# Kernel tuning notes

Hardware: AMD Instinct MI355X
Metric: run time of the kernel (lower is better)

The kernel has to match this reference:

```python
import jax, jax.numpy as jnp
import numpy as np
from jax import lax

N = 1_000_000   # nodes
E = 16_000_000  # edges
K1, K2, K3 = 100_000, 10_000, 2_500  # ceil(ratio*n) per pooling stage
EPS = 1e-5


def cgconv(x, src, dst, edge_attr, edge_valid, Wf, bf, Ws, bs, gamma, beta, num_nodes):
    # z_ij = [x_i, x_j, e_ij]  (PyG: i = target = dst, j = source = src)
    z = jnp.concatenate([x[dst], x[src], edge_attr], axis=-1)          # [E,3]
    m = jax.nn.sigmoid(z @ Wf + bf) * jax.nn.softplus(z @ Ws + bs)     # [E,1]
    m = m * edge_valid[:, None].astype(m.dtype)
    aggr = jax.ops.segment_sum(m, dst, num_segments=num_nodes)         # [n,1]
    # BatchNorm1d (training-mode batch stats, biased var), then residual
    mean = aggr.mean(axis=0)
    var = aggr.var(axis=0)
    bn = gamma * (aggr - mean) / jnp.sqrt(var + EPS) + beta
    return bn + x


def topk_pool(x, src, dst, edge_attr, edge_valid, w, k, num_nodes):
    # Original torch code broadcasts x[N,1]*w[C] -> sum(-1) == x*sum(w); tanh nonlinearity.
    score = jnp.tanh(x[:, 0] * jnp.sum(w) / jnp.linalg.norm(w))        # [n]
    top_scores, perm = lax.top_k(score, k)
    x_new = x[perm] * top_scores[:, None]
    mask = jnp.zeros((num_nodes,), bool).at[perm].set(True)
    new_idx = jnp.zeros((num_nodes,), jnp.int32).at[perm].set(jnp.arange(k, dtype=jnp.int32))
    ev = edge_valid & mask[src] & mask[dst]
    return x_new, new_idx[src], new_idx[dst], edge_attr, ev


def setup_inputs() -> dict:
    key = jax.random.key(0)
    ks = jax.random.split(key, 24)
    d = {}
    d["x"] = jax.random.normal(ks[0], (N, 1), jnp.float32)
    d["edge_attr"] = jax.random.uniform(ks[1], (E, 1), jnp.float32)
    d["src"] = jax.random.randint(ks[2], (E,), 0, N, jnp.int32)
    d["dst"] = jax.random.randint(ks[3], (E,), 0, N, jnp.int32)
    d["batch"] = jnp.zeros((N,), jnp.int32)
    p = lambda k, shp: jax.random.normal(k, shp, jnp.float32) * 0.1
    d["Wf1"], d["bf1"] = p(ks[4], (3, 1)), p(ks[5], (1,))
    d["Ws1"], d["bs1"] = p(ks[6], (3, 1)), p(ks[7], (1,))
    d["g1"], d["be1"] = jnp.ones((1,), jnp.float32), jnp.zeros((1,), jnp.float32)
    d["Wf2"], d["bf2"] = p(ks[8], (3, 1)), p(ks[9], (1,))
    d["Ws2"], d["bs2"] = p(ks[10], (3, 1)), p(ks[11], (1,))
    d["g2"], d["be2"] = jnp.ones((1,), jnp.float32), jnp.zeros((1,), jnp.float32)
    d["pw1"] = p(ks[12], (800,))
    d["pw2"] = p(ks[13], (80,))
    d["pw3"] = p(ks[14], (8,))
    d["Wl1"], d["bl1"] = p(ks[15], (1, 8)), p(ks[16], (8,))
    d["Wl2"], d["bl2"] = p(ks[17], (8, 2)), p(ks[18], (2,))
    return d


def reference(x, edge_attr, Wf1, bf1, Ws1, bs1, g1, be1, Wf2, bf2, Ws2, bs2, g2, be2,
              pw1, pw2, pw3, Wl1, bl1, Wl2, bl2, src, dst, batch):
    ev = jnp.ones((E,), bool)
    x = cgconv(x, src, dst, edge_attr, ev, Wf1, bf1, Ws1, bs1, g1, be1, N)
    x, s, dd, ea, ev = topk_pool(x, src, dst, edge_attr, ev, pw1, K1, N)
    x = cgconv(x, s, dd, ea, ev, Wf2, bf2, Ws2, bs2, g2, be2, K1)
    x, s, dd, ea, ev = topk_pool(x, s, dd, ea, ev, pw2, K2, K1)
    x, s, dd, ea, ev = topk_pool(x, s, dd, ea, ev, pw3, K3, K2)
    h = jax.nn.relu(x @ Wl1 + bl1)
    # dropout is identity in eval/reference mode
    return jax.nn.log_softmax(h @ Wl2 + bl2, axis=1)
```

## Files before the change

### kernel.cpp

```cpp
#include <hip/hip_runtime.h>
#include <math.h>

#define CHUNK 4096
#define NB2   256
#define BSH   12
#define CAP   24
#define CAPW  49
#define FG    16
#define RND   1024
#define EPB   16384

typedef int      i32x4 __attribute__((ext_vector_type(4)));
typedef float    f32x4 __attribute__((ext_vector_type(4)));
typedef unsigned u32x2 __attribute__((ext_vector_type(2)));
typedef unsigned u32x4 __attribute__((ext_vector_type(4)));

__device__ __forceinline__ i32x4 ntld4i(const int* p)   { return __builtin_nontemporal_load((const i32x4*)p); }
__device__ __forceinline__ f32x4 ntld4f(const float* p) { return __builtin_nontemporal_load((const f32x4*)p); }

__device__ __forceinline__ float sigmoidf_(float x) {
    if (x >= 0.0f) { float e = expf(-x); return 1.0f / (1.0f + e); }
    float e = expf(x); return e / (1.0f + e);
}
__device__ __forceinline__ float softplusf_(float x) {
    return fmaxf(x, 0.0f) + log1pf(expf(-fabsf(x)));
}
__device__ __forceinline__ unsigned key_desc(float f) {
    unsigned u = __float_as_uint(f);
    unsigned ka = (u & 0x80000000u) ? ~u : (u | 0x80000000u);
    return ~ka;
}
__device__ __forceinline__ float edge_m(float xd, float xs, float a,
                                        float wf0, float wf1, float wf2, float b0,
                                        float ws0, float ws1, float ws2, float b1) {
    float f = xd * wf0 + xs * wf1 + a * wf2 + b0;
    float g = xd * ws0 + xs * ws1 + a * ws2 + b1;
    return sigmoidf_(f) * softplusf_(g);
}

__global__ void k_consts(const float* __restrict__ pw1, const float* __restrict__ pw2,
                         const float* __restrict__ pw3, float* __restrict__ consts,
                         float* __restrict__ stats, unsigned* __restrict__ ghist,
                         int n1, int n2, int n3) {
    if (blockIdx.x == 0) {
        if (threadIdx.x < 16) stats[threadIdx.x] = 0.f;
        for (int i = threadIdx.x; i < 2048; i += 256) ghist[i] = 0u;
    }
    const float* w; int n;
    if (blockIdx.x == 0)      { w = pw1; n = n1; }
    else if (blockIdx.x == 1) { w = pw2; n = n2; }
    else                      { w = pw3; n = n3; }
    __shared__ float s1[256], s2[256];
    float a = 0.f, b = 0.f;
    for (int i = threadIdx.x; i < n; i += 256) { float v = w[i]; a += v; b += v * v; }
    s1[threadIdx.x] = a; s2[threadIdx.x] = b; __syncthreads();
    for (int o = 128; o > 0; o >>= 1) {
        if (threadIdx.x < o) { s1[threadIdx.x] += s1[threadIdx.x + o]; s2[threadIdx.x] += s2[threadIdx.x + o]; }
        __syncthreads();
    }
    if (threadIdx.x == 0) consts[blockIdx.x] = s1[0] / sqrtf(s2[0]);
}

__global__ void __launch_bounds__(256) k_ehist2(const int* __restrict__ dst,
                                                unsigned* __restrict__ hist,
                                                int e0, int e1) {
    __shared__ unsigned h[NB2];
    int t = threadIdx.x;
    h[t] = 0;
    __syncthreads();
    int cs = e0 + blockIdx.x * EPB;
    int ce = cs + EPB; if (ce > e1) ce = e1;
    for (int eb = cs; eb < ce; eb += RND) {
        int i = eb + t * 4;
        if (eb + RND <= ce) {
            i32x4 d4 = ntld4i(dst + i);
            atomicAdd(&h[((unsigned)d4.x) >> BSH], 1u);
            atomicAdd(&h[((unsigned)d4.y) >> BSH], 1u);
            atomicAdd(&h[((unsigned)d4.z) >> BSH], 1u);
// ... 130 lines not shown
    }
    for (int i = 0; i < NB2 / 16; ++i) {
        int b = sg + (i << 4);
        unsigned g = gcur[b], c = fil[b], ge = gend[b];
        unsigned* st = &stage[b * CAPW];
        for (unsigned p = g + ln; p < ge; p += 16) {
            unsigned k2 = p - g;
            rec[p] = (k2 < c) ? make_uint2(st[2 * k2], st[2 * k2 + 1]) : make_uint2(0u, 0u);
        }
    }
}

__global__ void __launch_bounds__(256) k_aggr2(
        const uint2* __restrict__ rec, const unsigned* __restrict__ tot,
        float* __restrict__ aggr, float* __restrict__ stats,
        int N, int accumulate, int doStats) {
    __shared__ float acc[1 << BSH];
    __shared__ unsigned sc[256];
    __shared__ unsigned sBase, sCnt;
    int t = threadIdx.x, b = blockIdx.x;
    {
        unsigned v = tot[t];
        sc[t] = v; __syncthreads();
        for (int o = 1; o < 256; o <<= 1) {
            unsigned u = (t >= o) ? sc[t - o] : 0u;
            __syncthreads();
            sc[t] += u; __syncthreads();
        }
        if (t == b) { sBase = sc[t] - v; sCnt = tot[t]; }
    }
    for (int i = t; i < (1 << BSH); i += 256) acc[i] = 0.f;
    __syncthreads();
    unsigned lo = sBase, hi = lo + sCnt;
    for (unsigned i = lo + t; i < hi; i += 256) {
        u32x2 r = __builtin_nontemporal_load((const u32x2*)&rec[i]);
        atomicAdd(&acc[r.y], __uint_as_float(r.x));
    }
    __syncthreads();
    int nb = b << BSH;
    float s = 0.f, q = 0.f;
    for (int i = t; i < (1 << BSH); i += 256) {
        int node = nb + i;
        if (node < N) {
            float v = acc[i];
            if (accumulate) v += aggr[node];
            aggr[node] = v;
            if (doStats) { s += v; q += v * v; }
        }
    }
    if (doStats) {
        __shared__ float s1[256], s2[256];
        s1[t] = s; s2[t] = q; __syncthreads();
        for (int o = 128; o > 0; o >>= 1) {
            if (t < o) { s1[t] += s1[t + o]; s2[t] += s2[t + o]; }
            __syncthreads();
        }
        if (t == 0) { atomicAdd(&stats[0], s1[0]); atomicAdd(&stats[1], s2[0]); }
    }
}

__global__ void k_conv1(const float* __restrict__ x, const float* __restrict__ ea,
                        const int* __restrict__ src, const int* __restrict__ dst,
                        const float* __restrict__ Wf, const float* __restrict__ bf,
                        const float* __restrict__ Ws, const float* __restrict__ bs,
                        float* __restrict__ aggr, int E) {
    int e = blockIdx.x * blockDim.x + threadIdx.x;
    if (e >= E) return;
    int s = src[e], d = dst[e];
    atomicAdd(&aggr[d], edge_m(x[d], x[s], ea[e], Wf[0], Wf[1], Wf[2], bf[0],
// ... 19 lines not shown
        s4[0]=sv.x; s4[1]=sv.y; s4[2]=sv.z; s4[3]=sv.w;
        cnt = 4;
    } else {
        cnt = E - base;
        for (int j = 0; j < cnt; ++j) { d4[j] = dst[base + j]; s4[j] = src[base + j]; }
    }
    #pragma unroll
    for (int j = 0; j < 4; ++j) {
        if (j >= cnt) break;
        int nd = nidx[d4[j]];
        if (nd < 0) continue;
        int ns = nidx[s4[j]];
        if (ns < 0) continue;
        float a = __builtin_nontemporal_load(ea + base + j);
        atomicAdd(&aggr[nd], edge_m(x2[nd], x2[ns], a, wf0, wf1, wf2, b0, ws0, ws1, ws2, b1));
    }
}

__global__ void k_stats(const float* __restrict__ a, int n, float* __restrict__ stats) {
    float s = 0.f, q = 0.f;
    int stride = gridDim.x * blockDim.x;
    for (int i = blockIdx.x * blockDim.x + threadIdx.x; i < n; i += stride) {
        float v = a[i]; s += v; q += v * v;
    }
    __shared__ float s1[256], s2[256];
    s1[threadIdx.x] = s; s2[threadIdx.x] = q; __syncthreads();
    for (int o = 128; o > 0; o >>= 1) {
        if (threadIdx.x < o) { s1[threadIdx.x] += s1[threadIdx.x + o]; s2[threadIdx.x] += s2[threadIdx.x + o]; }
        __syncthreads();
    }
    if (threadIdx.x == 0) { atomicAdd(&stats[0], s1[0]); atomicAdd(&stats[1], s2[0]); }
}

__global__ void k_bn(const float* __restrict__ aggr, const float* __restrict__ xin,
                     const float* __restrict__ stats, const float* __restrict__ g,
                     const float* __restrict__ be, float* __restrict__ xout,
                     int n, float invn, const float* __restrict__ consts, int ci,
                     unsigned* __restrict__ keys, unsigned* __restrict__ vals,
                     int* __restrict__ nidxInit, float* __restrict__ zeroArr, int nZero) {
    int i = blockIdx.x * blockDim.x + threadIdx.x;
    if (i >= n) return;
    if (nidxInit) nidxInit[i] = -1;
    if (zeroArr && i < nZero) zeroArr[i] = 0.f;
    float mean = stats[0] * invn;
    float var  = stats[1] * invn - mean * mean;
    float inv  = 1.0f / sqrtf(var + 1e-5f);
    float v = g[0] * (aggr[i] - mean) * inv + be[0] + xin[i];
    xout[i] = v;
    float s = tanhf(v * consts[ci]);
    keys[i] = key_desc(s);
    vals[i] = (unsigned)i;
}

__global__ void __launch_bounds__(256) k_ghist(const unsigned* __restrict__ keys,
                                               unsigned* __restrict__ ghist, int n) {
    __shared__ unsigned h[2048];
    int t = threadIdx.x;
    for (int i = t; i < 2048; i += 256) h[i] = 0;
    __syncthreads();
    int stride = gridDim.x * 1024;
    for (int base = blockIdx.x * 1024 + t * 4; base + 3 < n; base += stride) {
        u32x4 k4 = __builtin_nontemporal_load((const u32x4*)(keys + base));
        atomicAdd(&h[k4.x >> 21], 1u);
        atomicAdd(&h[k4.y >> 21], 1u);
        atomicAdd(&h[k4.z >> 21], 1u);
        atomicAdd(&h[k4.w >> 21], 1u);
    }
    if (blockIdx.x == 0) {
        int tail = n & ~3;
        for (int i = tail + t; i < n; i += 256)
            atomicAdd(&h[keys[i] >> 21], 1u);
    }
    __syncthreads();
    for (int i = t; i < 2048; i += 256) { unsigned v = h[i]; if (v) atomicAdd(&ghist[i], v); }
}

__global__ void k_findT(const unsigned* __restrict__ ghist, unsigned* __restrict__ sel, int K) {
    __shared__ unsigned s[256];
    int t = threadIdx.x;
    unsigned carry = 0;
    for (int tile = 0; tile < 8; ++tile) {
        unsigned v = ghist[tile * 256 + t];
        s[t] = v; __syncthreads();
        for (int o = 1; o < 256; o <<= 1) {
            unsigned u = (t >= o) ? s[t - o] : 0u;
            __syncthreads();
            s[t] += u; __syncthreads();
        }
        unsigned cum = s[t] + carry;
        if (cum >= (unsigned)K && cum - v < (unsigned)K) {
            sel[0] = (unsigned)(tile * 256 + t);
            sel[1] = cum;
        }
        unsigned tl = s[255]; __syncthreads();
        carry += tl;
    }
}

__global__ void __launch_bounds__(256) k_selcnt(const unsigned* __restrict__ keys,
                                                const unsigned* __restrict__ sel,
                                                unsigned* __restrict__ chist, int n) {
    unsigned T = sel[0];
    int t = threadIdx.x;
    int base = blockIdx.x * CHUNK;
    int end = base + CHUNK; if (end > n) end = n;
    unsigned c = 0;
    for (int i = base + t; i < end; i += 256)
        c += ((keys[i] >> 21) <= T) ? 1u : 0u;
    __shared__ unsigned s[256];
    s[t] = c; __syncthreads();
    for (int o = 128; o > 0; o >>= 1) { if (t < o) s[t] += s[t + o]; __syncthreads(); }
    if (t == 0) chist[blockIdx.x] = s[0];
}

__global__ void __launch_bounds__(256) k_selcompact(
        const unsigned* __restrict__ keys, const unsigned* __restrict__ vals,
        const unsigned* __restrict__ sel, const unsigned* __restrict__ chist,
        unsigned* __restrict__ okeys, unsigned* __restrict__ ovals, int n, int G) {
    __shared__ unsigned s[256];
    __shared__ unsigned wsum[4];
    __shared__ unsigned runS;
    unsigned T = sel[0];
    int t = threadIdx.x, wave = t >> 6, lane = t & 63;
    unsigned v = (t < G) ? chist[t] : 0u;
    s[t] = v; __syncthreads();
    for (int o = 1; o < 256; o <<= 1) {
        unsigned u = (t >= o) ? s[t - o] : 0u;
        __syncthreads();
        s[t] += u; __syncthreads();
    }
    if (t == (int)blockIdx.x) runS = s[t] - v;
    __syncthreads();
    int cbase = blockIdx.x * CHUNK;
    for (int gix = 0; gix < CHUNK / 256; ++gix) {
        int i = cbase + gix * 256 + t;
        bool selq = (i < n) && ((keys[i] >> 21) <= T);
        unsigned long long mk = __ballot(selq);
        unsigned pre = (unsigned)__popcll(mk & ((1ull << lane) - 1ull));
        if (lane == 0) wsum[wave] = (unsigned)__popcll(mk);
        __syncthreads();
        unsigned wb = runS;
        #pragma unroll
        for (int w = 0; w < 4; ++w) if (w < wave) wb += wsum[w];
        if (selq) { unsigned pos = wb + pre; okeys[pos] = keys[i]; ovals[pos] = vals[i]; }
        __syncthreads();
        if (t == 0) runS += wsum[0] + wsum[1] + wsum[2] + wsum[3];
        __syncthreads();
    }
}

__global__ void k_hist(const unsigned* __restrict__ keys, unsigned* __restrict__ hist,
                       int n, const unsigned* __restrict__ pn, int shift) {
    if (pn) n = (int)*pn;
    __shared__ unsigned h[256];
    int t = threadIdx.x;
    h[t] = 0;
    __syncthreads();
    int base = blockIdx.x * CHUNK;
    if (base + CHUNK <= n) {
        #pragma unroll
        for (int it = 0; it < CHUNK / 1024; ++it) {
            int i = base + it * 1024 + t * 4;
            const unsigned* p = keys + i;
            unsigned k0 = p[0], k1 = p[1], k2 = p[2], k3 = p[3];
            atomicAdd(&h[(k0 >> shift) & 255u], 1u);
            atomicAdd(&h[(k1 >> shift) & 255u], 1u);
            atomicAdd(&h[(k2 >> shift) & 255u], 1u);
            atomicAdd(&h[(k3 >> shift) & 255u], 1u);
        }
    } else {
        for (int i = base + t; i < n; i += 256)
            atomicAdd(&h[(keys[i] >> shift) & 255u], 1u);
    }
    __syncthreads();
    hist[blockIdx.x * 256 + t] = h[t];
}

__global__ void __launch_bounds__(256) k_scatter(const unsigned* __restrict__ keys,
                                                 const unsigned* __restrict__ vals,
                                                 unsigned* __restrict__ okeys,
                                                 unsigned* __restrict__ ovals,
                                                 const unsigned* __restrict__ offs,
                                                 const unsigned* __restrict__ tot,
                                                 int n, const unsigned* __restrict__ pn,
                                                 int shift) {
    if (pn) n = (int)*pn;
    if ((int)blockIdx.x * CHUNK >= n) return;
    __shared__ unsigned run[256];
    __shared__ unsigned offl[256];
    __shared__ unsigned wcnt[4][256];
    __shared__ unsigned wpre[4][256];
    __shared__ unsigned sc[256];
    int t = threadIdx.x;
    int wave = t >> 6, lane = t & 63;
    {
        unsigned v = tot[t];
        sc[t] = v; __syncthreads();
        for (int o = 1; o < 256; o <<= 1) {
            unsigned u = (t >= o) ? sc[t - o] : 0u;
            __syncthreads();
            sc[t] += u; __syncthreads();
        }
        offl[t] = offs[(size_t)blockIdx.x * 256 + t] + (sc[t] - v);
        run[t] = 0;
    }
    __syncthreads();
    int cbase = blockIdx.x * CHUNK;
    const int GROUPS = CHUNK / 256;
    for (int gix = 0; gix < GROUPS; ++gix) {
        int i = cbase + gix * 256 + t;
        bool active = i < n;
        unsigned k = active ? keys[i] : 0u;
        unsigned v = active ? vals[i] : 0u;
        unsigned d = (k >> shift) & 255u;
        unsigned long long amask = __ballot(active);
        unsigned long long bb[8];
        #pragma unroll
        for (int bit = 0; bit < 8; ++bit) bb[bit] = __ballot(active && ((d >> bit) & 1u));
        unsigned long long m = amask;
        #pragma unroll
        for (int bit = 0; bit < 8; ++bit) m &= ((d >> bit) & 1u) ? bb[bit] : ~bb[bit];
        unsigned rk = (unsigned)__popcll(m & ((1ull << lane) - 1ull));
        #pragma unroll
        for (int j = 0; j < 4; ++j) {
            unsigned dd = (unsigned)lane + j * 64u;
            unsigned long long mm = amask;
            #pragma unroll
            for (int bit = 0; bit < 8; ++bit) mm &= ((dd >> bit) & 1u) ? bb[bit] : ~bb[bit];
            wcnt[wave][dd] = (unsigned)__popcll(mm);
        }
        __syncthreads();
        {
            unsigned r = run[t];
            unsigned c0 = wcnt[0][t], c1 = wcnt[1][t], c2 = wcnt[2][t], c3 = wcnt[3][t];
            wpre[0][t] = r;
            wpre[1][t] = r + c0;
            wpre[2][t] = r + c0 + c1;
            wpre[3][t] = r + c0 + c1 + c2;
            run[t] = r + c0 + c1 + c2 + c3;
        }
        __syncthreads();
        if (active) {
            unsigned pos = offl[d] + wpre[wave][d] + rk;
            okeys[pos] = k;
            ovals[pos] = v;
        }
    }
}

__global__ void k_pool(const unsigned* __restrict__ perm, const float* __restrict__ xin,
                       const float* __restrict__ consts, int ci,
                       float* __restrict__ xout, int* __restrict__ newidx, int k,
                       unsigned* __restrict__ okeys, unsigned* __restrict__ ovals, int nci) {
    int r = blockIdx.x * blockDim.x + threadIdx.x;
    if (r >= k) return;
    unsigned p = perm[r];
    float xv = xin[p];
    float s = tanhf(xv * consts[ci]);
    float o = xv * s;
    xout[r] = o;
    if (newidx) newidx[p] = r;
    if (okeys) {
        float s2 = tanhf(o * consts[nci]);
        okeys[r] = key_desc(s2);
        ovals[r] = (unsigned)r;
    }
}

__global__ void __launch_bounds__(1024) k_smallsort(
        unsigned* __restrict__ kIn, unsigned* __restrict__ vIn,
        unsigned* __restrict__ kTmp, unsigned* __restrict__ vTmp,
        int n, int k3, const float* __restrict__ xin,
        const float* __restrict__ consts, int ci,
        const float* __restrict__ Wl1, const float* __restrict__ bl1,
        const float* __restrict__ Wl2, const float* __restrict__ bl2,
        float* __restrict__ out) {
    __shared__ unsigned hist[256], sc[256], run[256], offl[256];
    __shared__ unsigned wcnt[16][256];
    __shared__ unsigned wpre[16][256];
    int t = threadIdx.x;
    int wave = t >> 6, lane = t & 63;
    unsigned *ki = kIn, *vi = vIn, *ko = kTmp, *vo = vTmp;
    for (int p = 0; p < 4; ++p) {
        int shift = p * 8;
        if (t < 256) hist[t] = 0;
        __syncthreads();
        for (int i = t; i < n; i += 1024)
            atomicAdd(&hist[(ki[i] >> shift) & 255u], 1u);
        __syncthreads();
        if (t < 256) sc[t] = hist[t];
        __syncthreads();
        for (int o = 1; o < 256; o <<= 1) {
            unsigned u = 0;
            if (t < 256 && t >= o) u = sc[t - o];
            __syncthreads();
            if (t < 256) sc[t] += u;
            __syncthreads();
        }
// ... 33 lines not shown
            if (active) {
                unsigned pos = offl[d] + wpre[wave][d] + rk;
                ko[pos] = k;
                vo[pos] = v;
            }
            __syncthreads();
        }
        unsigned* tp;
        tp = ki; ki = ko; ko = tp;
        tp = vi; vi = vo; vo = tp;
        __syncthreads();
    }
    float c = consts[ci];
    float b20 = bl2[0], b21 = bl2[1];
    for (int r = t; r < k3; r += 1024) {
        unsigned pidx = vIn[r];
        float xv = xin[pidx];
        float s = tanhf(xv * c);
        float o = xv * s;
        float l0 = b20, l1 = b21;
        #pragma unroll
        for (int j = 0; j < 8; ++j) {
            float h = fmaxf(o * Wl1[j] + bl1[j], 0.0f);
            l0 += h * Wl2[2 * j];
            l1 += h * Wl2[2 * j + 1];
        }
        float mx = fmaxf(l0, l1);
        float lse = mx + logf(expf(l0 - mx) + expf(l1 - mx));
        out[2 * r]     = l0 - lse;
        out[2 * r + 1] = l1 - lse;
    }
}

static void sort_pairs(hipStream_t stream, unsigned* kI, unsigned* vI,
                       unsigned* kT, unsigned* vT, unsigned* hist, unsigned* offs,
                       unsigned* tot, int n, int G, const unsigned* pn) {
    unsigned *ki = kI, *vi = vI, *ko = kT, *vo = vT;
    for (int p = 0; p < 4; ++p) {
        int shift = p * 8;
        k_hist<<<G, 256, 0, stream>>>(ki, hist, n, pn, shift);
        k_scanA<<<256, 256, 0, stream>>>(hist, offs, tot, G, 0u);
        k_scatter<<<G, 256, 0, stream>>>(ki, vi, ko, vo, offs, tot, n, pn, shift);
        unsigned* t;
        t = ki; ki = ko; ko = t;
        t = vi; vi = vo; vo = t;
    }
}

extern "C" void kernel_launch(void* const* d_in, const int* in_sizes, int n_in,
                              void* d_out, int out_size, void* d_ws, size_t ws_size,
                              hipStream_t stream) {
    const float* x   = (const float*)d_in[0];
    const float* ea  = (const float*)d_in[1];
    const int*   src = (const int*)d_in[2];
    const int*   dst = (const int*)d_in[3];
    const float *Wf1 = (const float*)d_in[5],  *bf1 = (const float*)d_in[6];
    const float *Ws1 = (const float*)d_in[7],  *bs1 = (const float*)d_in[8];
    const float *g1  = (const float*)d_in[9],  *be1 = (const float*)d_in[10];
    const float *Wf2 = (const float*)d_in[11], *bf2 = (const float*)d_in[12];
    const float *Ws2 = (const float*)d_in[13], *bs2 = (const float*)d_in[14];
    const float *g2  = (const float*)d_in[15], *be2 = (const float*)d_in[16];
    const float *pw1 = (const float*)d_in[17], *pw2 = (const float*)d_in[18], *pw3 = (const float*)d_in[19];
    const float *Wl1 = (const float*)d_in[20], *bl1 = (const float*)d_in[21];
    const float *Wl2 = (const float*)d_in[22], *bl2 = (const float*)d_in[23];

    const int N  = in_sizes[0];
    const int E  = in_sizes[1];
    const int K1 = 100000, K2 = 10000, K3 = 2500;

    size_t off = 0;
    auto alloc = [&](size_t bytes) { size_t o = off; off = (off + bytes + 255) & ~(size_t)255; return o; };
    char* ws = (char*)d_ws;
    size_t o_x1    = alloc((size_t)N * 4);
    size_t o_nidx  = alloc((size_t)N * 4);
    size_t o_stats = alloc(256);
    size_t o_const = alloc(256);
    size_t o_tot   = alloc(4096);
    size_t o_gh    = alloc(8192);
    size_t o_x2    = alloc((size_t)K1 * 4);
    size_t o_x3    = alloc((size_t)K1 * 4);
    size_t o_ag2   = alloc((size_t)K1 * 4);
    size_t o_x4    = alloc((size_t)K2 * 4);
    size_t o_ag1   = alloc((size_t)N * 4);
    size_t o_arena = off;

    int G1 = (N + CHUNK - 1) / CHUNK;
    size_t s_kA = 0;
    size_t s_vA = s_kA + (((size_t)N * 4 + 255) & ~(size_t)255);
    size_t s_kB = s_vA + (((size_t)N * 4 + 255) & ~(size_t)255);
    size_t s_vB = s_kB + (((size_t)N * 4 + 255) & ~(size_t)255);
    size_t s_h  = s_vB + (((size_t)N * 4 + 255) & ~(size_t)255);
    size_t s_o  = s_h  + (((size_t)G1 * 256 * 4 + 255) & ~(size_t)255);
    size_t sortSz = s_o + (size_t)G1 * 256 * 4;

    int H = 0, Eh = 0;
    size_t p_rec = 0, p_eh = 0, p_eo = 0;
    for (int h = 1; h <= 8; h <<= 1) {
        int eh_ = (E + h - 1) / h;
        eh_ = (eh_ + RND - 1) & ~(RND - 1);
        int gc_ = (eh_ + EPB - 1) / EPB;
        size_t recB = (((size_t)eh_ + (size_t)gc_ * NB2 * FG + NB2 * FG) * 8 + 255) & ~(size_t)255;
        size_t ehB  = (((size_t)gc_ * NB2 * 4) + 255) & ~(size_t)255;
        size_t eoB  = (((size_t)gc_ * NB2 * 4) + 255) & ~(size_t)255;
        size_t partSz = recB + ehB + eoB;
        size_t arenaSz = partSz > sortSz ? partSz : sortSz;
        if (o_arena + arenaSz <= ws_size && N <= (NB2 << BSH)) {
            H = h; Eh = eh_;
            p_rec = 0; p_eh = p_rec + recB; p_eo = p_eh + ehB;
            break;
        }
    }

    float*    x1     = (float*)(ws + o_x1);
    int*      nidx   = (int*)(ws + o_nidx);
    float*    stats  = (float*)(ws + o_stats);
    float*    consts = (float*)(ws + o_const);
    unsigned* tot    = (unsigned*)(ws + o_tot);
    unsigned* selp   = tot + 512;
    unsigned* ghist  = (unsigned*)(ws + o_gh);
    float*    x2     = (float*)(ws + o_x2);
    float*    x3     = (float*)(ws + o_x3);
    float*    aggr2  = (float*)(ws + o_ag2);
    float*    x4     = (float*)(ws + o_x4);
    float*    aggr1  = (float*)(ws + o_ag1);
    unsigned* kA     = (unsigned*)(ws + o_arena + s_kA);
    unsigned* vA     = (unsigned*)(ws + o_arena + s_vA);
    unsigned* kB     = (unsigned*)(ws + o_arena + s_kB);
    unsigned* vB     = (unsigned*)(ws + o_arena + s_vB);
    unsigned* hist   = (unsigned*)(ws + o_arena + s_h);
    unsigned* offs   = (unsigned*)(ws + o_arena + s_o);

    k_consts<<<3, 256, 0, stream>>>(pw1, pw2, pw3, consts, stats, ghist,
                                    in_sizes[17], in_sizes[18], in_sizes[19]);

    if (H > 0) {
        uint2*    rec = (uint2*)(ws + o_arena + p_rec);
        unsigned* eh  = (unsigned*)(ws + o_arena + p_eh);
        unsigned* eo  = (unsigned*)(ws + o_arena + p_eo);
        int NBN = (N + (1 << BSH) - 1) >> BSH;
        for (int h = 0; h < H; ++h) {
            int e0 = h * Eh;
            int e1 = e0 + Eh; if (e1 > E) e1 = E;
            if (e0 >= e1) break;
            int GCh = (e1 - e0 + EPB - 1) / EPB;
            k_ehist2<<<GCh, 256, 0, stream>>>(dst, eh, e0, e1);
            k_scanA<<<NB2, 256, 0, stream>>>(eh, eo, tot, GCh, (unsigned)(FG - 1));
            k_part<<<GCh, 256, 0, stream>>>(x, ea, src, dst, Wf1, bf1, Ws1, bs1,
                                            eo, tot, eh, rec, e0, e1);
            k_aggr2<<<NBN, 256, 0, stream>>>(rec, tot, aggr1, stats, N,
                                             h > 0, h == H - 1 ? 1 : 0);
        }
    } else {
        hipMemsetAsync(aggr1, 0, (size_t)N * 4, stream);
        k_conv1<<<(E + 255) / 256, 256, 0, stream>>>(x, ea, src, dst, Wf1, bf1, Ws1, bs1, aggr1, E);
        k_stats<<<1024, 256, 0, stream>>>(aggr1, N, stats);
    }
    k_bn<<<(N + 255) / 256, 256, 0, stream>>>(aggr1, x, stats, g1, be1, x1, N, 1.0f / (float)N,
                                              consts, 0, kA, vA, nidx, aggr2, K1);

    k_ghist<<<256, 256, 0, stream>>>(kA, ghist, N);
    k_findT<<<1, 256, 0, stream>>>(ghist, selp, K1);
    k_selcnt<<<G1, 256, 0, stream>>>(kA, selp, hist, N);
    k_selcompact<<<G1, 256, 0, stream>>>(kA, vA, selp, hist, kB, vB, N, G1);
    sort_pairs(stream, kB, vB, kA, vA, hist, offs, tot, N, G1, selp + 1);
    k_pool<<<(K1 + 255) / 256, 256, 0, stream>>>(vB, x1, consts, 0, x2, nidx, K1,
                                                 (unsigned*)nullptr, (unsigned*)nullptr, 0);

    k_conv2<<<(E / 4 + 255) / 256, 256, 0, stream>>>(x2, ea, src, dst, nidx,
                                                     Wf2, bf2, Ws2, bs2, aggr2, E);
    k_stats<<<256, 256, 0, stream>>>(aggr2, K1, stats + 2);
    k_bn<<<(K1 + 255) / 256, 256, 0, stream>>>(aggr2, x2, stats + 2, g2, be2, x3, K1, 1.0f / (float)K1,
                                               consts, 1, kA, vA,
                                               (int*)nullptr, (float*)nullptr, 0);

    sort_pairs(stream, kA, vA, kB, vB, hist, offs, tot, K1,
               (K1 + CHUNK - 1) / CHUNK, (const unsigned*)nullptr);
    k_pool<<<(K2 + 255) / 256, 256, 0, stream>>>(vA, x3, consts, 1, x4, (int*)nullptr, K2,
                                                 kB, vB, 2);

    k_smallsort<<<1, 1024, 0, stream>>>(kB, vB, kA, vA, K2, K3, x4, consts, 2,
                                        Wl1, bl1, Wl2, bl2, (float*)d_out);
}
```

Before: 845.7 us.

## Fuse selection and radix sort passes into persistent kernels with grid barriers

Replaces the chain of small launches (batch norm, global histogram, threshold find, select count, compaction, and four hist/scan/scatter radix passes plus pooling) with three persistent kernels that synchronise through a software grid barrier built on atomics. Each sort block now computes its digit offsets by reading every block's histogram directly, which removes the separate scan kernel and the offs buffer. It also changes the bucket capacity constants and has the aggregation loop read two records per 16-byte load. The aim is to cut launch overhead and inter-kernel gaps. In exchange it relies on all blocks of each grid being resident at once, since otherwise the spin barrier deadlocks, and each sort pass now does a redundant per-block sweep over all block histograms.

```diff
diff --git a/kernel.cpp b/kernel.cpp
--- a/kernel.cpp
+++ b/kernel.cpp
@@ -4,8 +4,8 @@
 #define CHUNK 4096
 #define NB2   256
 #define BSH   12
-#define CAP   24
-#define CAPW  49
+#define CAP   20
+#define CAPW  41
 #define FG    16
 #define RND   1024
 #define EPB   16384
@@ -38,12 +38,28 @@
     return sigmoidf_(f) * softplusf_(g);
 }
 
+__device__ __forceinline__ void gridbar(unsigned* cnt, unsigned* ep, unsigned G) {
+    __syncthreads();
+    __threadfence();
+    if (threadIdx.x == 0) {
+        __hip_atomic_fetch_add(cnt, 1u, __ATOMIC_ACQ_REL, __HIP_MEMORY_SCOPE_AGENT);
+        unsigned tgt = (*ep + 1u) * G;
+        while (__hip_atomic_load(cnt, __ATOMIC_ACQUIRE, __HIP_MEMORY_SCOPE_AGENT) < tgt)
+            __builtin_amdgcn_s_sleep(8);
+    }
+    ++(*ep);
+    __syncthreads();
+    __threadfence();
+}
+
 __global__ void k_consts(const float* __restrict__ pw1, const float* __restrict__ pw2,
                          const float* __restrict__ pw3, float* __restrict__ consts,
                          float* __restrict__ stats, unsigned* __restrict__ ghist,
+                         unsigned* __restrict__ cnts,
                          int n1, int n2, int n3) {
     if (blockIdx.x == 0) {
         if (threadIdx.x < 16) stats[threadIdx.x] = 0.f;
+        if (threadIdx.x < 8)  cnts[threadIdx.x] = 0u;
         for (int i = threadIdx.x; i < 2048; i += 256) ghist[i] = 0u;
     }
     const float* w; int n;
@@ -240,9 +256,10 @@
     for (int i = t; i < (1 << BSH); i += 256) acc[i] = 0.f;
     __syncthreads();
     unsigned lo = sBase, hi = lo + sCnt;
-    for (unsigned i = lo + t; i < hi; i += 256) {
-        u32x2 r = __builtin_nontemporal_load((const u32x2*)&rec[i]);
+    for (unsigned i = lo + 2 * t; i < hi; i += 512) {
+        u32x4 r = __builtin_nontemporal_load((const u32x4*)&rec[i]);
         atomicAdd(&acc[r.y], __uint_as_float(r.x));
+        atomicAdd(&acc[r.w], __uint_as_float(r.z));
     }
     __syncthreads();
     int nb = b << BSH;
@@ -328,238 +345,252 @@
     if (threadIdx.x == 0) { atomicAdd(&stats[0], s1[0]); atomicAdd(&stats[1], s2[0]); }
 }
 
-__global__ void k_bn(const float* __restrict__ aggr, const float* __restrict__ xin,
-                     const float* __restrict__ stats, const float* __restrict__ g,
-                     const float* __restrict__ be, float* __restrict__ xout,
-                     int n, float invn, const float* __restrict__ consts, int ci,
-                     unsigned* __restrict__ keys, unsigned* __restrict__ vals,
-                     int* __restrict__ nidxInit, float* __restrict__ zeroArr, int nZero) {
-    int i = blockIdx.x * blockDim.x + threadIdx.x;
-    if (i >= n) return;
-    if (nidxInit) nidxInit[i] = -1;
-    if (zeroArr && i < nZero) zeroArr[i] = 0.f;
-    float mean = stats[0] * invn;
-    float var  = stats[1] * invn - mean * mean;
-    float inv  = 1.0f / sqrtf(var + 1e-5f);
-    float v = g[0] * (aggr[i] - mean) * inv + be[0] + xin[i];
-    xout[i] = v;
-    float s = tanhf(v * consts[ci]);
-    keys[i] = key_desc(s);
-    vals[i] = (unsigned)i;
-}
-
-__global__ void __launch_bounds__(256) k_ghist(const unsigned* __restrict__ keys,
-                                               unsigned* __restrict__ ghist, int n) {
-    __shared__ unsigned h[2048];
-    int t = threadIdx.x;
-    for (int i = t; i < 2048; i += 256) h[i] = 0;
-    __syncthreads();
-    int stride = gridDim.x * 1024;
-    for (int base = blockIdx.x * 1024 + t * 4; base + 3 < n; base += stride) {
-        u32x4 k4 = __builtin_nontemporal_load((const u32x4*)(keys + base));
-        atomicAdd(&h[k4.x >> 21], 1u);
-        atomicAdd(&h[k4.y >> 21], 1u);
-        atomicAdd(&h[k4.z >> 21], 1u);
-        atomicAdd(&h[k4.w >> 21], 1u);
-    }
-    if (blockIdx.x == 0) {
-        int tail = n & ~3;
-        for (int i = tail + t; i < n; i += 256)
-            atomicAdd(&h[keys[i] >> 21], 1u);
-    }
-    __syncthreads();
-    for (int i = t; i < 2048; i += 256) { unsigned v = h[i]; if (v) atomicAdd(&ghist[i], v); }
-}
-
-__global__ void k_findT(const unsigned* __restrict__ ghist, unsigned* __restrict__ sel, int K) {
-    __shared__ unsigned s[256];
-    int t = threadIdx.x;
-    unsigned carry = 0;
-    for (int tile = 0; tile < 8; ++tile) {
-        unsigned v = ghist[tile * 256 + t];
-        s[t] = v; __syncthreads();
-        for (int o = 1; o < 256; o <<= 1) {
-            unsigned u = (t >= o) ? s[t - o] : 0u;
-            __syncthreads();
-            s[t] += u; __syncthreads();
-        }
-        unsigned cum = s[t] + carry;
-        if (cum >= (unsigned)K && cum - v < (unsigned)K) {
-            sel[0] = (unsigned)(tile * 256 + t);
-            sel[1] = cum;
-        }
-        unsigned tl = s[255]; __syncthreads();
-        carry += tl;
-    }
-}
-
-__global__ void __launch_bounds__(256) k_selcnt(const unsigned* __restrict__ keys,
-                                                const unsigned* __restrict__ sel,
-                                                unsigned* __restrict__ chist, int n) {
-    unsigned T = sel[0];
-    int t = threadIdx.x;
-    int base = blockIdx.x * CHUNK;
-    int end = base + CHUNK; if (end > n) end = n;
-    unsigned c = 0;
-    for (int i = base + t; i < end; i += 256)
-        c += ((keys[i] >> 21) <= T) ? 1u : 0u;
-    __shared__ unsigned s[256];
-    s[t] = c; __syncthreads();
-    for (int o = 128; o > 0; o >>= 1) { if (t < o) s[t] += s[t + o]; __syncthreads(); }
-    if (t == 0) chist[blockIdx.x] = s[0];
-}
-
-__global__ void __launch_bounds__(256) k_selcompact(
-        const unsigned* __restrict__ keys, const unsigned* __restrict__ vals,
-        const unsigned* __restrict__ sel, const unsigned* __restrict__ chist,
-        unsigned* __restrict__ okeys, unsigned* __restrict__ ovals, int n, int G) {
-    __shared__ unsigned s[256];
+__global__ void __launch_bounds__(256) k_select(
+        const float* __restrict__ aggr1, const float* __restrict__ x,
+        const float* __restrict__ stats, const float* __restrict__ g1,
+        const float* __restrict__ be1, const float* __restrict__ consts,
+        float* __restrict__ x1, unsigned* __restrict__ keys, unsigned* __restrict__ vals,
+        int* __restrict__ nidx, float* __restrict__ aggr2, int K1, int N, float invn,
+        unsigned* __restrict__ ghist, unsigned* __restrict__ sel,
+        unsigned* __restrict__ chist, unsigned* __restrict__ okeys,
+        unsigned* __restrict__ ovals, unsigned* __restrict__ cnt, int Gc) {
+    __shared__ unsigned h2[2048];
+    __shared__ unsigned fs[256];
     __shared__ unsigned wsum[4];
     __shared__ unsigned runS;
+    unsigned ep = 0;
+    int t = threadIdx.x, b = blockIdx.x;
+    unsigned G = gridDim.x;
+    for (int i = t; i < 2048; i += 256) h2[i] = 0;
+    __syncthreads();
+    {
+        float mean = stats[0] * invn;
+        float var  = stats[1] * invn - mean * mean;
+        float rinv = 1.0f / sqrtf(var + 1e-5f);
+        float gg = g1[0], bb = be1[0], c0 = consts[0];
+        int gid = b * 256 + t, gsz = (int)G * 256;
+        for (int i = gid; i < N; i += gsz) {
+            float v = gg * (aggr1[i] - mean) * rinv + bb + x[i];
+            x1[i] = v;
+            unsigned k = key_desc(tanhf(v * c0));
+            keys[i] = k;
+            vals[i] = (unsigned)i;
+            nidx[i] = -1;
+            if (i < K1) aggr2[i] = 0.f;
+            atomicAdd(&h2[k >> 21], 1u);
+        }
+    }
+    __syncthreads();
+    for (int i = t; i < 2048; i += 256) { unsigned v = h2[i]; if (v) atomicAdd(&ghist[i], v); }
+    gridbar(cnt, &ep, G);
+    if (b == 0) {
+        unsigned carry = 0;
+        int K = K1;
+        for (int tile = 0; tile < 8; ++tile) {
+            unsigned v = ghist[tile * 256 + t];
+            fs[t] = v; __syncthreads();
+            for (int o = 1; o < 256; o <<= 1) {
+                unsigned u = (t >= o) ? fs[t - o] : 0u;
+                __syncthreads();
+                fs[t] += u; __syncthreads();
+            }
+            unsigned cum = fs[t] + carry;
+            if (cum >= (unsigned)K && cum - v < (unsigned)K) {
+                sel[0] = (unsigned)(tile * 256 + t);
+                sel[1] = cum;
+            }
+            unsigned tl = fs[255]; __syncthreads();
+            carry += tl;
+        }
+    }
+    gridbar(cnt, &ep, G);
     unsigned T = sel[0];
-    int t = threadIdx.x, wave = t >> 6, lane = t & 63;
-    unsigned v = (t < G) ? chist[t] : 0u;
-    s[t] = v; __syncthreads();
-    for (int o = 1; o < 256; o <<= 1) {
-        unsigned u = (t >= o) ? s[t - o] : 0u;
-        __syncthreads();
-        s[t] += u; __syncthreads();
-    }
-    if (t == (int)blockIdx.x) runS = s[t] - v;
-    __syncthreads();
-    int cbase = blockIdx.x * CHUNK;
-    for (int gix = 0; gix < CHUNK / 256; ++gix) {
-        int i = cbase + gix * 256 + t;
-        bool selq = (i < n) && ((keys[i] >> 21) <= T);
-        unsigned long long mk = __ballot(selq);
-        unsigned pre = (unsigned)__popcll(mk & ((1ull << lane) - 1ull));
-        if (lane == 0) wsum[wave] = (unsigned)__popcll(mk);
-        __syncthreads();
-        unsigned wb = runS;
-        #pragma unroll
-        for (int w = 0; w < 4; ++w) if (w < wave) wb += wsum[w];
-        if (selq) { unsigned pos = wb + pre; okeys[pos] = keys[i]; ovals[pos] = vals[i]; }
-        __syncthreads();
-        if (t == 0) runS += wsum[0] + wsum[1] + wsum[2] + wsum[3];
-        __syncthreads();
-    }
-}
-
-__global__ void k_hist(const unsigned* __restrict__ keys, unsigned* __restrict__ hist,
-                       int n, const unsigned* __restrict__ pn, int shift) {
-    if (pn) n = (int)*pn;
-    __shared__ unsigned h[256];
-    int t = threadIdx.x;
-    h[t] = 0;
-    __syncthreads();
-    int base = blockIdx.x * CHUNK;
-    if (base + CHUNK <= n) {
-        #pragma unroll
-        for (int it = 0; it < CHUNK / 1024; ++it) {
-            int i = base + it * 1024 + t * 4;
-            const unsigned* p = keys + i;
-            unsigned k0 = p[0], k1 = p[1], k2 = p[2], k3 = p[3];
-            atomicAdd(&h[(k0 >> shift) & 255u], 1u);
-            atomicAdd(&h[(k1 >> shift) & 255u], 1u);
-            atomicAdd(&h[(k2 >> shift) & 255u], 1u);
-            atomicAdd(&h[(k3 >> shift) & 255u], 1u);
-        }
-    } else {
-        for (int i = base + t; i < n; i += 256)
-            atomicAdd(&h[(keys[i] >> shift) & 255u], 1u);
-    }
-    __syncthreads();
-    hist[blockIdx.x * 256 + t] = h[t];
-}
-
-__global__ void __launch_bounds__(256) k_scatter(const unsigned* __restrict__ keys,
-                                                 const unsigned* __restrict__ vals,
-                                                 unsigned* __restrict__ okeys,
-                                                 unsigned* __restrict__ ovals,
-                                                 const unsigned* __restrict__ offs,
-                                                 const unsigned* __restrict__ tot,
-                                                 int n, const unsigned* __restrict__ pn,
-                                                 int shift) {
-    if (pn) n = (int)*pn;
-    if ((int)blockIdx.x * CHUNK >= n) return;
-    __shared__ unsigned run[256];
-    __shared__ unsigned offl[256];
-    __shared__ unsigned wcnt[4][256];
-    __shared__ unsigned wpre[4][256];
-    __shared__ unsigned sc[256];
-    int t = threadIdx.x;
+    if (b < Gc) {
+        int base = b * CHUNK;
+        int end = base + CHUNK; if (end > N) end = N;
+        unsigned c = 0;
+        for (int i = base + t; i < end; i += 256)
+            c += ((keys[i] >> 21) <= T) ? 1u : 0u;
+        fs[t] = c; __syncthreads();
+        for (int o = 128; o > 0; o >>= 1) { if (t < o) fs[t] += fs[t + o]; __syncthreads(); }
+        if (t == 0) chist[b] = fs[0];
+    }
+    gridbar(cnt, &ep, G);
+    if (b < Gc) {
+        unsigned partial = 0;
+        for (int g = t; g < b; g += 256) partial += chist[g];
+        fs[t] = partial; __syncthreads();
+        for (int o = 128; o > 0; o >>= 1) { if (t < o) fs[t] += fs[t + o]; __syncthreads(); }
+        if (t == 0) runS = fs[0];
+        __syncthreads();
+        int wave = t >> 6, lane = t & 63;
+        int cbase = b * CHUNK;
+        for (int gix = 0; gix < CHUNK / 256; ++gix) {
+            int i = cbase + gix * 256 + t;
+            bool selq = (i < N) && ((keys[i] >> 21) <= T);
+            unsigned long long mk = __ballot(selq);
+            unsigned pre = (unsigned)__popcll(mk & ((1ull << lane) - 1ull));
+            if (lane == 0) wsum[wave] = (unsigned)__popcll(mk);
+            __syncthreads();
+            unsigned wb = runS;
+            #pragma unroll
+            for (int w = 0; w < 4; ++w) if (w < wave) wb += wsum[w];
+            if (selq) { unsigned pos = wb + pre; okeys[pos] = keys[i]; ovals[pos] = vals[i]; }
+            __syncthreads();
+            if (t == 0) runS += wsum[0] + wsum[1] + wsum[2] + wsum[3];
+            __syncthreads();
+        }
+    }
+}
+
+__device__ __forceinline__ void msort_body(unsigned*& ki, unsigned*& vi,
+                                           unsigned*& ko, unsigned*& vo,
+                                           int n, unsigned* hist,
+                                           unsigned* cnt, unsigned* ep) {
+    __shared__ unsigned h[256], offl[256], run[256], sc[256];
+    __shared__ unsigned wcnt[4][256], wpre[4][256];
+    int t = threadIdx.x, b = blockIdx.x;
+    unsigned G = gridDim.x;
     int wave = t >> 6, lane = t & 63;
-    {
-        unsigned v = tot[t];
-        sc[t] = v; __syncthreads();
+    for (int p = 0; p < 4; ++p) {
+        int shift = p * 8;
+        h[t] = 0;
+        __syncthreads();
+        int base = b * CHUNK;
+        if (base + CHUNK <= n) {
+            #pragma unroll
+            for (int it = 0; it < CHUNK / 1024; ++it) {
+                int i = base + it * 1024 + t * 4;
+                const unsigned* pk = ki + i;
+                atomicAdd(&h[(pk[0] >> shift) & 255u], 1u);
+                atomicAdd(&h[(pk[1] >> shift) & 255u], 1u);
+                atomicAdd(&h[(pk[2] >> shift) & 255u], 1u);
+                atomicAdd(&h[(pk[3] >> shift) & 255u], 1u);
+            }
+        } else {
+            for (int i = base + t; i < n; i += 256)
+                atomicAdd(&h[(ki[i] >> shift) & 255u], 1u);
+        }
+        __syncthreads();
+        hist[(size_t)b * 256 + t] = h[t];
+        gridbar(cnt, ep, G);
+        unsigned pre = 0, totd = 0;
+        for (int g = 0; g < (int)G; ++g) {
+            unsigned v = hist[(size_t)g * 256 + t];
+            pre += (g < b) ? v : 0u;
+            totd += v;
+        }
+        sc[t] = totd; __syncthreads();
         for (int o = 1; o < 256; o <<= 1) {
             unsigned u = (t >= o) ? sc[t - o] : 0u;
             __syncthreads();
             sc[t] += u; __syncthreads();
         }
-        offl[t] = offs[(size_t)blockIdx.x * 256 + t] + (sc[t] - v);
+        offl[t] = (sc[t] - totd) + pre;
         run[t] = 0;
-    }
-    __syncthreads();
-    int cbase = blockIdx.x * CHUNK;
-    const int GROUPS = CHUNK / 256;
-    for (int gix = 0; gix < GROUPS; ++gix) {
-        int i = cbase + gix * 256 + t;
-        bool active = i < n;
-        unsigned k = active ? keys[i] : 0u;
-        unsigned v = active ? vals[i] : 0u;
-        unsigned d = (k >> shift) & 255u;
-        unsigned long long amask = __ballot(active);
-        unsigned long long bb[8];
-        #pragma unroll
-        for (int bit = 0; bit < 8; ++bit) bb[bit] = __ballot(active && ((d >> bit) & 1u));
-        unsigned long long m = amask;
-        #pragma unroll
-        for (int bit = 0; bit < 8; ++bit) m &= ((d >> bit) & 1u) ? bb[bit] : ~bb[bit];
-        unsigned rk = (unsigned)__popcll(m & ((1ull << lane) - 1ull));
-        #pragma unroll
-        for (int j = 0; j < 4; ++j) {
-            unsigned dd = (unsigned)lane + j * 64u;
-            unsigned long long mm = amask;
-            #pragma unroll
-            for (int bit = 0; bit < 8; ++bit) mm &= ((dd >> bit) & 1u) ? bb[bit] : ~bb[bit];
-            wcnt[wave][dd] = (unsigned)__popcll(mm);
-        }
-        __syncthreads();
-        {
-            unsigned r = run[t];
-            unsigned c0 = wcnt[0][t], c1 = wcnt[1][t], c2 = wcnt[2][t], c3 = wcnt[3][t];
-            wpre[0][t] = r;
-            wpre[1][t] = r + c0;
-            wpre[2][t] = r + c0 + c1;
-            wpre[3][t] = r + c0 + c1 + c2;
-            run[t] = r + c0 + c1 + c2 + c3;
-        }
-        __syncthreads();
-        if (active) {
-            unsigned pos = offl[d] + wpre[wave][d] + rk;
-            okeys[pos] = k;
-            ovals[pos] = v;
-        }
-    }
-}
-
-__global__ void k_pool(const unsigned* __restrict__ perm, const float* __restrict__ xin,
-                       const float* __restrict__ consts, int ci,
-                       float* __restrict__ xout, int* __restrict__ newidx, int k,
-                       unsigned* __restrict__ okeys, unsigned* __restrict__ ovals, int nci) {
-    int r = blockIdx.x * blockDim.x + threadIdx.x;
-    if (r >= k) return;
-    unsigned p = perm[r];
-    float xv = xin[p];
-    float s = tanhf(xv * consts[ci]);
-    float o = xv * s;
-    xout[r] = o;
-    if (newidx) newidx[p] = r;
-    if (okeys) {
-        float s2 = tanhf(o * consts[nci]);
-        okeys[r] = key_desc(s2);
-        ovals[r] = (unsigned)r;
+        __syncthreads();
+        if (base < n) {
+            for (int gix = 0; gix < CHUNK / 256; ++gix) {
+                int i = base + gix * 256 + t;
+                bool active = i < n;
+                unsigned k = active ? ki[i] : 0u;
+                unsigned v = active ? vi[i] : 0u;
+                unsigned d = (k >> shift) & 255u;
+                unsigned long long amask = __ballot(active);
+                unsigned long long bb[8];
+                #pragma unroll
+                for (int bit = 0; bit < 8; ++bit) bb[bit] = __ballot(active && ((d >> bit) & 1u));
+                unsigned long long m = amask;
+                #pragma unroll
+                for (int bit = 0; bit < 8; ++bit) m &= ((d >> bit) & 1u) ? bb[bit] : ~bb[bit];
+                unsigned rk = (unsigned)__popcll(m & ((1ull << lane) - 1ull));
+                #pragma unroll
+                for (int j = 0; j < 4; ++j) {
+                    unsigned dd = (unsigned)lane + j * 64u;
+                    unsigned long long mm = amask;
+                    #pragma unroll
+                    for (int bit = 0; bit < 8; ++bit) mm &= ((dd >> bit) & 1u) ? bb[bit] : ~bb[bit];
+                    wcnt[wave][dd] = (unsigned)__popcll(mm);
+                }
+                __syncthreads();
+                {
+                    unsigned r = run[t];
+                    unsigned c0 = wcnt[0][t], c1 = wcnt[1][t], c2 = wcnt[2][t], c3 = wcnt[3][t];
+                    wpre[0][t] = r;
+                    wpre[1][t] = r + c0;
+                    wpre[2][t] = r + c0 + c1;
+                    wpre[3][t] = r + c0 + c1 + c2;
+                    run[t] = r + c0 + c1 + c2 + c3;
+                }
+                __syncthreads();
+                if (active) {
+                    unsigned pos = offl[d] + wpre[wave][d] + rk;
+                    ko[pos] = k;
+                    vo[pos] = v;
+                }
+            }
+        }
+        gridbar(cnt, ep, G);
+        unsigned* tp;
+        tp = ki; ki = ko; ko = tp;
+        tp = vi; vi = vo; vo = tp;
+    }
+}
+
+__global__ void __launch_bounds__(256) k_msort1(
+        unsigned* kIn, unsigned* vIn, unsigned* kTmp, unsigned* vTmp,
+        const unsigned* __restrict__ pn, unsigned* hist, unsigned* cnt,
+        const float* __restrict__ x1, const float* __restrict__ consts,
+        float* __restrict__ x2, int* __restrict__ nidx, int K1) {
+    unsigned ep = 0;
+    int n = (int)*pn;
+    unsigned *ki = kIn, *vi = vIn, *ko = kTmp, *vo = vTmp;
+    msort_body(ki, vi, ko, vo, n, hist, cnt, &ep);
+    float c = consts[0];
+    int gid = blockIdx.x * 256 + threadIdx.x, gsz = gridDim.x * 256;
+    for (int r = gid; r < K1; r += gsz) {
+        unsigned p = vi[r];
+        float xv = x1[p];
+        float s = tanhf(xv * c);
+        x2[r] = xv * s;
+        nidx[p] = r;
+    }
+}
+
+__global__ void __launch_bounds__(256) k_msort2(
+        unsigned* kIn, unsigned* vIn, unsigned* kTmp, unsigned* vTmp,
+        int n, unsigned* hist, unsigned* cnt,
+        const float* __restrict__ aggr2, const float* __restrict__ x2,
+        const float* __restrict__ stats2, const float* __restrict__ g2,
+        const float* __restrict__ be2, const float* __restrict__ consts,
+        float* __restrict__ x3, float* __restrict__ x4, int K2, float invn) {
+    unsigned ep = 0;
+    unsigned G = gridDim.x;
+    {
+        float mean = stats2[0] * invn;
+        float var  = stats2[1] * invn - mean * mean;
+        float rinv = 1.0f / sqrtf(var + 1e-5f);
+        float gg = g2[0], bb = be2[0], c1 = consts[1];
+        int gid = blockIdx.x * 256 + threadIdx.x, gsz = (int)G * 256;
+        for (int i = gid; i < n; i += gsz) {
+            float v = gg * (aggr2[i] - mean) * rinv + bb + x2[i];
+            x3[i] = v;
+            kIn[i] = key_desc(tanhf(v * c1));
+            vIn[i] = (unsigned)i;
+        }
+    }
+    gridbar(cnt, &ep, G);
+    unsigned *ki = kIn, *vi = vIn, *ko = kTmp, *vo = vTmp;
+    msort_body(ki, vi, ko, vo, n, hist, cnt, &ep);
+    float c1 = consts[1], c2 = consts[2];
+    int gid = blockIdx.x * 256 + threadIdx.x, gsz = (int)G * 256;
+    for (int r = gid; r < K2; r += gsz) {
+        unsigned p = vi[r];
+        float xv = x3[p];
+        float o = xv * tanhf(xv * c1);
+        x4[r] = o;
+        kTmp[r] = key_desc(tanhf(o * c2));
+        vTmp[r] = (unsigned)r;
     }
 }
 
@@ -659,21 +690,6 @@
     }
 }
 
-static void sort_pairs(hipStream_t stream, unsigned* kI, unsigned* vI,
-                       unsigned* kT, unsigned* vT, unsigned* hist, unsigned* offs,
-                       unsigned* tot, int n, int G, const unsigned* pn) {
-    unsigned *ki = kI, *vi = vI, *ko = kT, *vo = vT;
-    for (int p = 0; p < 4; ++p) {
-        int shift = p * 8;
-        k_hist<<<G, 256, 0, stream>>>(ki, hist, n, pn, shift);
-        k_scanA<<<256, 256, 0, stream>>>(hist, offs, tot, G, 0u);
-        k_scatter<<<G, 256, 0, stream>>>(ki, vi, ko, vo, offs, tot, n, pn, shift);
-        unsigned* t;
-        t = ki; ki = ko; ko = t;
-        t = vi; vi = vo; vo = t;
-    }
-}
-
 extern "C" void kernel_launch(void* const* d_in, const int* in_sizes, int n_in,
                               void* d_out, int out_size, void* d_ws, size_t ws_size,
                               hipStream_t stream) {
@@ -702,7 +718,7 @@
     size_t o_nidx  = alloc((size_t)N * 4);
     size_t o_stats = alloc(256);
     size_t o_const = alloc(256);
-    size_t o_tot   = alloc(4096);
+    size_t o_tot   = alloc(8192);
     size_t o_gh    = alloc(8192);
     size_t o_x2    = alloc((size_t)K1 * 4);
     size_t o_x3    = alloc((size_t)K1 * 4);
@@ -717,8 +733,7 @@
     size_t s_kB = s_vA + (((size_t)N * 4 + 255) & ~(size_t)255);
     size_t s_vB = s_kB + (((size_t)N * 4 + 255) & ~(size_t)255);
     size_t s_h  = s_vB + (((size_t)N * 4 + 255) & ~(size_t)255);
-    size_t s_o  = s_h  + (((size_t)G1 * 256 * 4 + 255) & ~(size_t)255);
-    size_t sortSz = s_o + (size_t)G1 * 256 * 4;
+    size_t sortSz = s_h + (size_t)G1 * 256 * 4;
 
     int H = 0, Eh = 0;
     size_t p_rec = 0, p_eh = 0, p_eo = 0;
@@ -744,6 +759,7 @@
     float*    consts = (float*)(ws + o_const);
     unsigned* tot    = (unsigned*)(ws + o_tot);
     unsigned* selp   = tot + 512;
+    unsigned* cnts   = tot + 768;
     unsigned* ghist  = (unsigned*)(ws + o_gh);
     float*    x2     = (float*)(ws + o_x2);
     float*    x3     = (float*)(ws + o_x3);
@@ -755,9 +771,8 @@
     unsigned* kB     = (unsigned*)(ws + o_arena + s_kB);
     unsigned* vB     = (unsigned*)(ws + o_arena + s_vB);
     unsigned* hist   = (unsigned*)(ws + o_arena + s_h);
-    unsigned* offs   = (unsigned*)(ws + o_arena + s_o);
-
-    k_consts<<<3, 256, 0, stream>>>(pw1, pw2, pw3, consts, stats, ghist,
+
+    k_consts<<<3, 256, 0, stream>>>(pw1, pw2, pw3, consts, stats, ghist, cnts,
                                     in_sizes[17], in_sizes[18], in_sizes[19]);
 
     if (H > 0) {
@@ -782,28 +797,21 @@
         k_conv1<<<(E + 255) / 256, 256, 0, stream>>>(x, ea, src, dst, Wf1, bf1, Ws1, bs1, aggr1, E);
         k_stats<<<1024, 256, 0, stream>>>(aggr1, N, stats);
     }
-    k_bn<<<(N + 255) / 256, 256, 0, stream>>>(aggr1, x, stats, g1, be1, x1, N, 1.0f / (float)N,
-                                              consts, 0, kA, vA, nidx, aggr2, K1);
-
-    k_ghist<<<256, 256, 0, stream>>>(kA, ghist, N);
-    k_findT<<<1, 256, 0, stream>>>(ghist, selp, K1);
-    k_selcnt<<<G1, 256, 0, stream>>>(kA, selp, hist, N);
-    k_selcompact<<<G1, 256, 0, stream>>>(kA, vA, selp, hist, kB, vB, N, G1);
-    sort_pairs(stream, kB, vB, kA, vA, hist, offs, tot, N, G1, selp + 1);
-    k_pool<<<(K1 + 255) / 256, 256, 0, stream>>>(vB, x1, consts, 0, x2, nidx, K1,
-                                                 (unsigned*)nullptr, (unsigned*)nullptr, 0);
+
+    k_select<<<256, 256, 0, stream>>>(aggr1, x, stats, g1, be1, consts,
+                                      x1, kA, vA, nidx, aggr2, K1, N, 1.0f / (float)N,
+                                      ghist, selp, hist, kB, vB, cnts + 0, G1);
+
+    k_msort1<<<G1, 256, 0, stream>>>(kB, vB, kA, vA, selp + 1, hist, cnts + 1,
+                                     x1, consts, x2, nidx, K1);
 
     k_conv2<<<(E / 4 + 255) / 256, 256, 0, stream>>>(x2, ea, src, dst, nidx,
                                                      Wf2, bf2, Ws2, bs2, aggr2, E);
     k_stats<<<256, 256, 0, stream>>>(aggr2, K1, stats + 2);
-    k_bn<<<(K1 + 255) / 256, 256, 0, stream>>>(aggr2, x2, stats + 2, g2, be2, x3, K1, 1.0f / (float)K1,
-                                               consts, 1, kA, vA,
-                                               (int*)nullptr, (float*)nullptr, 0);
-
-    sort_pairs(stream, kA, vA, kB, vB, hist, offs, tot, K1,
-               (K1 + CHUNK - 1) / CHUNK, (const unsigned*)nullptr);
-    k_pool<<<(K2 + 255) / 256, 256, 0, stream>>>(vA, x3, consts, 1, x4, (int*)nullptr, K2,
-                                                 kB, vB, 2);
+
+    k_msort2<<<(K1 + CHUNK - 1) / CHUNK, 256, 0, stream>>>(
+        kA, vA, kB, vB, K1, hist, cnts + 2,
+        aggr2, x2, stats + 2, g2, be2, consts, x3, x4, K2, 1.0f / (float)K1);
 
     k_smallsort<<<1, 1024, 0, stream>>>(kB, vB, kA, vA, K2, K3, x4, consts, 2,
                                         Wl1, bl1, Wl2, bl2, (float*)d_out);
```

Result: slower. 1.714 ms (+102.7%).

## Fold radix-sort scan into scatter kernel and vectorize record aggregation loads

Applied to the files above, without the earlier changes.

Removes the separate k_scanA launch from each radix sort pass. Each scatter block now recomputes its digit prefix and totals by looping over all chunk histograms, which saves one launch per pass at the cost of redundant reads. The aggregation kernel now reads two edge records per 16-byte load. It also shrinks the CAP/CAPW constants and adds an early exit in k_hist for chunks beyond the selected count. The paired record loads rely on the segment start being even and the count being handled; an odd boundary could be misaligned or read past the segment.

```diff
diff --git a/kernel.cpp b/kernel.cpp
--- a/kernel.cpp
+++ b/kernel.cpp
@@ -4,8 +4,8 @@
 #define CHUNK 4096
 #define NB2   256
 #define BSH   12
-#define CAP   24
-#define CAPW  49
+#define CAP   20
+#define CAPW  41
 #define FG    16
 #define RND   1024
 #define EPB   16384
@@ -240,9 +240,10 @@
     for (int i = t; i < (1 << BSH); i += 256) acc[i] = 0.f;
     __syncthreads();
     unsigned lo = sBase, hi = lo + sCnt;
-    for (unsigned i = lo + t; i < hi; i += 256) {
-        u32x2 r = __builtin_nontemporal_load((const u32x2*)&rec[i]);
+    for (unsigned i = lo + 2 * t; i < hi; i += 512) {
+        u32x4 r = __builtin_nontemporal_load((const u32x4*)&rec[i]);
         atomicAdd(&acc[r.y], __uint_as_float(r.x));
+        atomicAdd(&acc[r.w], __uint_as_float(r.z));
     }
     __syncthreads();
     int nb = b << BSH;
@@ -448,11 +449,12 @@
 __global__ void k_hist(const unsigned* __restrict__ keys, unsigned* __restrict__ hist,
                        int n, const unsigned* __restrict__ pn, int shift) {
     if (pn) n = (int)*pn;
+    int base = blockIdx.x * CHUNK;
+    if (base >= n) return;
     __shared__ unsigned h[256];
     int t = threadIdx.x;
     h[t] = 0;
     __syncthreads();
-    int base = blockIdx.x * CHUNK;
     if (base + CHUNK <= n) {
         #pragma unroll
         for (int it = 0; it < CHUNK / 1024; ++it) {
@@ -469,19 +471,20 @@
             atomicAdd(&h[(keys[i] >> shift) & 255u], 1u);
     }
     __syncthreads();
-    hist[blockIdx.x * 256 + t] = h[t];
+    hist[(size_t)blockIdx.x * 256 + t] = h[t];
 }
 
 __global__ void __launch_bounds__(256) k_scatter(const unsigned* __restrict__ keys,
                                                  const unsigned* __restrict__ vals,
                                                  unsigned* __restrict__ okeys,
                                                  unsigned* __restrict__ ovals,
-                                                 const unsigned* __restrict__ offs,
-                                                 const unsigned* __restrict__ tot,
+                                                 const unsigned* __restrict__ hist,
                                                  int n, const unsigned* __restrict__ pn,
                                                  int shift) {
     if (pn) n = (int)*pn;
-    if ((int)blockIdx.x * CHUNK >= n) return;
+    int b = blockIdx.x;
+    int nch = (n + CHUNK - 1) / CHUNK;
+    if (b >= nch) return;
     __shared__ unsigned run[256];
     __shared__ unsigned offl[256];
     __shared__ unsigned wcnt[4][256];
@@ -490,18 +493,23 @@
     int t = threadIdx.x;
     int wave = t >> 6, lane = t & 63;
     {
-        unsigned v = tot[t];
-        sc[t] = v; __syncthreads();
+        unsigned pre = 0, totd = 0;
+        for (int c = 0; c < nch; ++c) {
+            unsigned v = hist[(size_t)c * 256 + t];
+            totd += v;
+            if (c < b) pre += v;
+        }
+        sc[t] = totd; __syncthreads();
         for (int o = 1; o < 256; o <<= 1) {
             unsigned u = (t >= o) ? sc[t - o] : 0u;
             __syncthreads();
             sc[t] += u; __syncthreads();
         }
-        offl[t] = offs[(size_t)blockIdx.x * 256 + t] + (sc[t] - v);
+        offl[t] = (sc[t] - totd) + pre;
         run[t] = 0;
     }
     __syncthreads();
-    int cbase = blockIdx.x * CHUNK;
+    int cbase = b * CHUNK;
     const int GROUPS = CHUNK / 256;
     for (int gix = 0; gix < GROUPS; ++gix) {
         int i = cbase + gix * 256 + t;
@@ -660,14 +668,13 @@
 }
 
 static void sort_pairs(hipStream_t stream, unsigned* kI, unsigned* vI,
-                       unsigned* kT, unsigned* vT, unsigned* hist, unsigned* offs,
-                       unsigned* tot, int n, int G, const unsigned* pn) {
+                       unsigned* kT, unsigned* vT, unsigned* hist,
+                       int n, int G, const unsigned* pn) {
     unsigned *ki = kI, *vi = vI, *ko = kT, *vo = vT;
     for (int p = 0; p < 4; ++p) {
         int shift = p * 8;
         k_hist<<<G, 256, 0, stream>>>(ki, hist, n, pn, shift);
-        k_scanA<<<256, 256, 0, stream>>>(hist, offs, tot, G, 0u);
-        k_scatter<<<G, 256, 0, stream>>>(ki, vi, ko, vo, offs, tot, n, pn, shift);
+        k_scatter<<<G, 256, 0, stream>>>(ki, vi, ko, vo, hist, n, pn, shift);
         unsigned* t;
         t = ki; ki = ko; ko = t;
         t = vi; vi = vo; vo = t;
@@ -717,8 +724,7 @@
     size_t s_kB = s_vA + (((size_t)N * 4 + 255) & ~(size_t)255);
     size_t s_vB = s_kB + (((size_t)N * 4 + 255) & ~(size_t)255);
     size_t s_h  = s_vB + (((size_t)N * 4 + 255) & ~(size_t)255);
-    size_t s_o  = s_h  + (((size_t)G1 * 256 * 4 + 255) & ~(size_t)255);
-    size_t sortSz = s_o + (size_t)G1 * 256 * 4;
+    size_t sortSz = s_h + (size_t)G1 * 256 * 4;
 
     int H = 0, Eh = 0;
     size_t p_rec = 0, p_eh = 0, p_eo = 0;
@@ -755,7 +761,6 @@
     unsigned* kB     = (unsigned*)(ws + o_arena + s_kB);
     unsigned* vB     = (unsigned*)(ws + o_arena + s_vB);
     unsigned* hist   = (unsigned*)(ws + o_arena + s_h);
-    unsigned* offs   = (unsigned*)(ws + o_arena + s_o);
 
     k_consts<<<3, 256, 0, stream>>>(pw1, pw2, pw3, consts, stats, ghist,
                                     in_sizes[17], in_sizes[18], in_sizes[19]);
@@ -789,7 +794,7 @@
     k_findT<<<1, 256, 0, stream>>>(ghist, selp, K1);
     k_selcnt<<<G1, 256, 0, stream>>>(kA, selp, hist, N);
     k_selcompact<<<G1, 256, 0, stream>>>(kA, vA, selp, hist, kB, vB, N, G1);
-    sort_pairs(stream, kB, vB, kA, vA, hist, offs, tot, N, G1, selp + 1);
+    sort_pairs(stream, kB, vB, kA, vA, hist, N, G1, selp + 1);
     k_pool<<<(K1 + 255) / 256, 256, 0, stream>>>(vB, x1, consts, 0, x2, nidx, K1,
                                                  (unsigned*)nullptr, (unsigned*)nullptr, 0);
 
@@ -800,7 +805,7 @@
                                                consts, 1, kA, vA,
                                                (int*)nullptr, (float*)nullptr, 0);
 
-    sort_pairs(stream, kA, vA, kB, vB, hist, offs, tot, K1,
+    sort_pairs(stream, kA, vA, kB, vB, hist, K1,
                (K1 + CHUNK - 1) / CHUNK, (const unsigned*)nullptr);
     k_pool<<<(K2 + 255) / 256, 256, 0, stream>>>(vA, x3, consts, 1, x4, (int*)nullptr, K2,
                                                  kB, vB, 2);
```

After: 932.6 us. +10.3%, slower.
